# Optimization experiments

Hardware: AMD Instinct MI355X
Metric: run time of the kernel (lower is better)

Reference implementation:

```python
import jax, jax.numpy as jnp
import numpy as np

DIM = 1024
NUM_HEADS = 16
HEAD_DIM = DIM // NUM_HEADS
HIDDEN = 2 * DIM  # swiglu hidden


def rotate_half(x):
    x1, x2 = jnp.split(x, 2, axis=-1)
    return jnp.concatenate((-x2, x1), axis=-1)


def setup_inputs() -> dict:
    key = jax.random.key(0)
    ks = jax.random.split(key, 9)
    s = lambda fan_in: 1.0 / np.sqrt(fan_in)
    x = jax.random.normal(ks[0], (4, 2048, DIM), dtype=jnp.float32)
    qkv_w = jax.random.uniform(ks[1], (3 * DIM, DIM), minval=-s(DIM), maxval=s(DIM))
    proj_w = jax.random.uniform(ks[2], (DIM, DIM), minval=-s(DIM), maxval=s(DIM))
    proj_b = jax.random.uniform(ks[3], (DIM,), minval=-s(DIM), maxval=s(DIM))
    w1_w = jax.random.uniform(ks[4], (HIDDEN, DIM), minval=-s(DIM), maxval=s(DIM))
    w1_b = jnp.zeros((HIDDEN,), jnp.float32)
    w2_w = jax.random.uniform(ks[5], (HIDDEN, DIM), minval=-s(DIM), maxval=s(DIM))
    w2_b = jnp.zeros((HIDDEN,), jnp.float32)
    w3_w = jax.random.uniform(ks[6], (DIM, HIDDEN), minval=-s(HIDDEN), maxval=s(HIDDEN))
    w3_b = jnp.zeros((DIM,), jnp.float32)
    return {"x": x, "qkv_w": qkv_w, "proj_w": proj_w, "proj_b": proj_b,
            "w1_w": w1_w, "w1_b": w1_b, "w2_w": w2_w, "w2_b": w2_b,
            "w3_w": w3_w, "w3_b": w3_b}


def reference(x, qkv_w, proj_w, proj_b, w1_w, w1_b, w2_w, w2_b, w3_w, w3_b):
    B, N, C = x.shape
    H, D = NUM_HEADS, HEAD_DIM
    scale = D ** -0.5
    # QKV projection (no bias)
    qkv = jnp.einsum('bnc,fc->bnf', x, qkv_w).reshape(B, N, 3, H, D)
    qkv = jnp.transpose(qkv, (2, 0, 3, 1, 4))  # [3, B, H, N, D]
    q, k, v = qkv[0], qkv[1], qkv[2]
    # Rotary embeddings
    inv_freq = 1.0 / (10000.0 ** (jnp.arange(0, D, 2, dtype=jnp.float32) / D))
    t = jnp.arange(N, dtype=jnp.float32)
    freqs = jnp.einsum('i,j->ij', t, inv_freq)
    emb = jnp.concatenate((freqs, freqs), axis=-1)[None, None]  # [1,1,N,D]
    cos, sin = jnp.cos(emb), jnp.sin(emb)
    q = q * cos + rotate_half(q) * sin
    k = k * cos + rotate_half(k) * sin
    # Attention (non-causal, as in source)
    attn = jnp.einsum('bhnd,bhmd->bhnm', q, k) * scale
    attn = jax.nn.softmax(attn, axis=-1)
    out = jnp.einsum('bhnm,bhmd->bhnd', attn, v)
    out = jnp.transpose(out, (0, 2, 1, 3)).reshape(B, N, C)
    out = jnp.einsum('bnc,fc->bnf', out, proj_w) + proj_b
    # SwiGLU MLP
    x1 = jnp.einsum('bnc,fc->bnf', out, w1_w) + w1_b
    x2 = jnp.einsum('bnc,fc->bnf', out, w2_w) + w2_b
    hidden = jax.nn.silu(x1) * x2
    return jnp.einsum('bnh,fh->bnf', hidden, w3_w) + w3_b
```

## Files before the change

### kernel.cpp

```cpp
#include <hip/hip_runtime.h>
#include <hip/hip_bf16.h>
#include <math.h>


#define SEQ     2048
#define BATCH   4
#define NH      16
#define CDIM    1024
#define MROWS   8192

typedef __bf16 bf16x8 __attribute__((ext_vector_type(8)));
typedef float  floatx4 __attribute__((ext_vector_type(4)));
typedef float  floatx16 __attribute__((ext_vector_type(16)));
typedef unsigned int u32;

__device__ __forceinline__ unsigned short f2bf(float f) {
    __bf16 h = (__bf16)f;
    return __builtin_bit_cast(unsigned short, h);
}
__device__ __forceinline__ float fexp2(float x) {
    float r; asm("v_exp_f32 %0, %1" : "=v"(r) : "v"(x)); return r;
}
__device__ __forceinline__ float frcp(float x) {
    float r; asm("v_rcp_f32 %0, %1" : "=v"(r) : "v"(x)); return r;
}
__device__ __forceinline__ u32 cvtpk(float lo, float hi) {
    u32 w; asm("v_cvt_pk_bf16_f32 %0, %1, %2" : "=v"(w) : "v"(lo), "v"(hi));
    return w;
}
__device__ __forceinline__ floatx4 mfma16(bf16x8 a, bf16x8 b, floatx4 c) {
    return __builtin_amdgcn_mfma_f32_16x16x32_bf16(a, b, c, 0, 0, 0);
}
__device__ __forceinline__ floatx16 mfma32(bf16x8 a, bf16x8 b, floatx16 c) {
    return __builtin_amdgcn_mfma_f32_32x32x16_bf16(a, b, c, 0, 0, 0);
}
__device__ __forceinline__ void gld16(void* lds, const void* g) {
    __builtin_amdgcn_global_load_lds(
        (const __attribute__((address_space(1))) u32*)g,
        (__attribute__((address_space(3))) u32*)lds, 16, 0, 0);
}
__device__ __forceinline__ void wait_vm0_barrier() {
    asm volatile("s_waitcnt vmcnt(0)" ::: "memory");
    __builtin_amdgcn_s_barrier();
    __builtin_amdgcn_sched_barrier(0);
}
__device__ __forceinline__ void raw_barrier() {
    __builtin_amdgcn_s_barrier();
    __builtin_amdgcn_sched_barrier(0);
}

template <int OUTMODE, bool BIAS>
__global__ __launch_bounds__(256) void mgemm(
    const unsigned short* __restrict__ A,
    const unsigned short* __restrict__ B,
    const float* __restrict__ bias,
    void* __restrict__ C, int ldc,
    int K)
{
    __shared__ __align__(16) unsigned short As[2][128 * 32];
    __shared__ __align__(16) unsigned short Bs[2][128 * 32];

    const int tid  = threadIdx.x;
    const int lane = tid & 63;
    const int wave = tid >> 6;
    const int l16  = lane & 15;
    const int quad = lane >> 4;
    const int wm = (wave >> 1) * 64, wn = (wave & 1) * 64;
    const int bm = blockIdx.y, bn = blockIdx.x;

    const unsigned short* Ag = A + (size_t)(bm * 128) * K;
    const unsigned short* Bg = B + (size_t)(bn * 128) * K;

    const int srow0 = wave * 32 + (lane >> 2);
    const int scol  = (lane & 3) * 8;
    const unsigned short* gA0 = Ag + (size_t)srow0 * K + scol;
    const unsigned short* gA1 = Ag + (size_t)(srow0 + 16) * K + scol;
    const unsigned short* gB0 = Bg + (size_t)srow0 * K + scol;
    const unsigned short* gB1 = Bg + (size_t)(srow0 + 16) * K + scol;

    auto stage = [&](int b, int kt) {
        gld16(&As[b][(wave * 2 + 0) * 512], gA0 + kt);
        gld16(&As[b][(wave * 2 + 1) * 512], gA1 + kt);
        gld16(&Bs[b][(wave * 2 + 0) * 512], gB0 + kt);
        gld16(&Bs[b][(wave * 2 + 1) * 512], gB1 + kt);
    };

    floatx4 acc[4][4] = {};
    const int NK = K >> 5;

    stage(0, 0);
    wait_vm0_barrier();

    for (int i = 0; i < NK; ++i) {
        const int cur = i & 1;
        if (i + 1 < NK) stage(cur ^ 1, (i + 1) * 32);

        bf16x8 af[4], bfr[4];
        #pragma unroll
        for (int mt = 0; mt < 4; ++mt)
            af[mt] = *(const bf16x8*)&As[cur][(wm + mt * 16 + l16) * 32 + quad * 8];
        #pragma unroll
        for (int nt = 0; nt < 4; ++nt)
            bfr[nt] = *(const bf16x8*)&Bs[cur][(wn + nt * 16 + l16) * 32 + quad * 8];
        #pragma unroll
        for (int mt = 0; mt < 4; ++mt)
            #pragma unroll
            for (int nt = 0; nt < 4; ++nt)
                acc[mt][nt] = mfma16(af[mt], bfr[nt], acc[mt][nt]);

        if (i + 1 < NK) wait_vm0_barrier();
        else            raw_barrier();
    }

    #pragma unroll
    for (int nt = 0; nt < 4; ++nt) {
        const int gcol = bn * 128 + wn + nt * 16 + l16;
        const float bv = BIAS ? bias[gcol] : 0.0f;
        #pragma unroll
        for (int mt = 0; mt < 4; ++mt) {
            #pragma unroll
            for (int r = 0; r < 4; ++r) {
                const int grow = bm * 128 + wm + mt * 16 + quad * 4 + r;
                float v = acc[mt][nt][r] + bv;
                if (OUTMODE == 0)
                    ((float*)C)[(size_t)grow * ldc + gcol] = v;
                else
                    ((unsigned short*)C)[(size_t)grow * ldc + gcol] = f2bf(v);
            }
        }
    }
}

__global__ __launch_bounds__(256) void mgemm_glu(
    const unsigned short* __restrict__ A,
    const unsigned short* __restrict__ B1,
    const unsigned short* __restrict__ B2,
    const float* __restrict__ bias1,
    const float* __restrict__ bias2,
    unsigned short* __restrict__ C, int ldc,
    int K)
{
    __shared__ __align__(16) unsigned short As[2][128 * 32];
    __shared__ __align__(16) unsigned short B1s[2][64 * 32];
    __shared__ __align__(16) unsigned short B2s[2][64 * 32];

    const int tid  = threadIdx.x;
    const int lane = tid & 63;
    const int wave = tid >> 6;
    const int l16  = lane & 15;
    const int quad = lane >> 4;
    const int wm = (wave >> 1) * 64, wn = (wave & 1) * 32;
    const int bm = blockIdx.y, bn = blockIdx.x;

    const unsigned short* Ag  = A  + (size_t)(bm * 128) * K;
    const unsigned short* B1g = B1 + (size_t)(bn * 64) * K;
    const unsigned short* B2g = B2 + (size_t)(bn * 64) * K;

    const int arow = wave * 32 + (lane >> 2);
    const int brow = wave * 16 + (lane >> 2);
    const int scol = (lane & 3) * 8;
    const unsigned short* gA0 = Ag  + (size_t)arow * K + scol;
    const unsigned short* gA1 = Ag  + (size_t)(arow + 16) * K + scol;
    const unsigned short* gB1 = B1g + (size_t)brow * K + scol;
    const unsigned short* gB2 = B2g + (size_t)brow * K + scol;

    auto stage = [&](int b, int kt) {
        gld16(&As[b][(wave * 2 + 0) * 512], gA0 + kt);
        gld16(&As[b][(wave * 2 + 1) * 512], gA1 + kt);
        gld16(&B1s[b][wave * 512], gB1 + kt);
        gld16(&B2s[b][wave * 512], gB2 + kt);
    };

    floatx4 acc1[4][2] = {};
    floatx4 acc2[4][2] = {};
    const int NK = K >> 5;

    stage(0, 0);
    wait_vm0_barrier();

    for (int i = 0; i < NK; ++i) {
        const int cur = i & 1;
        if (i + 1 < NK) stage(cur ^ 1, (i + 1) * 32);

        bf16x8 af[4], b1f[2], b2f[2];
        #pragma unroll
        for (int mt = 0; mt < 4; ++mt)
            af[mt] = *(const bf16x8*)&As[cur][(wm + mt * 16 + l16) * 32 + quad * 8];
        #pragma unroll
        for (int nt = 0; nt < 2; ++nt) {
            b1f[nt] = *(const bf16x8*)&B1s[cur][(wn + nt * 16 + l16) * 32 + quad * 8];
            b2f[nt] = *(const bf16x8*)&B2s[cur][(wn + nt * 16 + l16) * 32 + quad * 8];
        }
        #pragma unroll
        for (int mt = 0; mt < 4; ++mt)
            #pragma unroll
            for (int nt = 0; nt < 2; ++nt) {
                acc1[mt][nt] = mfma16(af[mt], b1f[nt], acc1[mt][nt]);
                acc2[mt][nt] = mfma16(af[mt], b2f[nt], acc2[mt][nt]);
            }

        if (i + 1 < NK) wait_vm0_barrier();
        else            raw_barrier();
    }

    #pragma unroll
    for (int nt = 0; nt < 2; ++nt) {
        const int gcol = bn * 64 + wn + nt * 16 + l16;
        const float b1 = bias1[gcol];
        const float b2 = bias2[gcol];
        #pragma unroll
        for (int mt = 0; mt < 4; ++mt) {
            #pragma unroll
            for (int r = 0; r < 4; ++r) {
                const int grow = bm * 128 + wm + mt * 16 + quad * 4 + r;
                const float x1 = acc1[mt][nt][r] + b1;
                const float x2 = acc2[mt][nt][r] + b2;
                const float e = fexp2(x1 * -1.44269504088896f);
                const float v = x1 * frcp(1.0f + e) * x2;
                C[(size_t)grow * ldc + gcol] = f2bf(v);
            }
        }
    }
}

__global__ __launch_bounds__(256) void mgemm_qkv(
    const unsigned short* __restrict__ A,
    const unsigned short* __restrict__ B,
    const float* __restrict__ tab,
    unsigned short* __restrict__ Qb,
    unsigned short* __restrict__ Kb,
    unsigned short* __restrict__ Vtb)
{
    __shared__ __align__(16) unsigned short As[2][128 * 32];
    __shared__ __align__(16) unsigned short Bs[2][128 * 32];

    const int tid  = threadIdx.x;
    const int lane = tid & 63;
    const int wave = tid >> 6;
    const int l16  = lane & 15;
    const int quad = lane >> 4;
    const int wm = (wave >> 1) * 64, wn = (wave & 1) * 64;
    const int bm = blockIdx.y, bn = blockIdx.x;
    const int K = CDIM;

    const unsigned short* Ag = A + (size_t)(bm * 128) * K;
    const unsigned short* Bg = B + (size_t)(bn * 128) * K;

    const int srow0 = wave * 32 + (lane >> 2);
    const int scol  = (lane & 3) * 8;
    const unsigned short* gA0 = Ag + (size_t)srow0 * K + scol;
    const unsigned short* gA1 = Ag + (size_t)(srow0 + 16) * K + scol;
    const unsigned short* gB0 = Bg + (size_t)srow0 * K + scol;
    const unsigned short* gB1 = Bg + (size_t)(srow0 + 16) * K + scol;

    auto stage = [&](int b, int kt) {
        gld16(&As[b][(wave * 2 + 0) * 512], gA0 + kt);
        gld16(&As[b][(wave * 2 + 1) * 512], gA1 + kt);
        gld16(&Bs[b][(wave * 2 + 0) * 512], gB0 + kt);
        gld16(&Bs[b][(wave * 2 + 1) * 512], gB1 + kt);
    };

    floatx4 acc[4][4] = {};
    const int NK = K >> 5;

    stage(0, 0);
    wait_vm0_barrier();

    for (int i = 0; i < NK; ++i) {
        const int cur = i & 1;
        if (i + 1 < NK) stage(cur ^ 1, (i + 1) * 32);

        bf16x8 af[4], bfr[4];
        #pragma unroll
        for (int mt = 0; mt < 4; ++mt)
            af[mt] = *(const bf16x8*)&As[cur][(wm + mt * 16 + l16) * 32 + quad * 8];
        #pragma unroll
        for (int nt = 0; nt < 4; ++nt)
            bfr[nt] = *(const bf16x8*)&Bs[cur][(wn + nt * 16 + l16) * 32 + quad * 8];
        #pragma unroll
        for (int mt = 0; mt < 4; ++mt)
            #pragma unroll
            for (int nt = 0; nt < 4; ++nt)
                acc[mt][nt] = mfma16(af[mt], bfr[nt], acc[mt][nt]);

        if (i + 1 < NK) wait_vm0_barrier();
        else            raw_barrier();
    }

    const int colbase0 = bn * 128;
    const int part = colbase0 >> 10;

    if (part == 2) {
        unsigned short* T = &As[0][0];
        #pragma unroll
        for (int mt = 0; mt < 4; ++mt) {
            __syncthreads();
            #pragma unroll
            for (int nt = 0; nt < 4; ++nt) {
                ushort4 pk;
                pk.x = f2bf(acc[mt][nt][0]); pk.y = f2bf(acc[mt][nt][1]);
                pk.z = f2bf(acc[mt][nt][2]); pk.w = f2bf(acc[mt][nt][3]);
                *(ushort4*)&T[((wave * 64 + nt * 16 + l16) * 16) + quad * 4] = pk;
            }
            __syncthreads();
            const int w2 = tid >> 6, d = tid & 63;
            const int nrow0 = bm * 128 + (w2 >> 1) * 64 + mt * 16;
            const int b = nrow0 >> 11, n0 = nrow0 & 2047;
            const int h2 = ((bn * 128 + (w2 & 1) * 64) & 1023) >> 6;
            unsigned short* dst = Vtb +
                ((size_t)(b * NH + h2) * 64 + d) * 2048 + n0;
            const int tb = (w2 * 64 + d) * 16;
            *(uint4*)dst       = *(const uint4*)&T[tb];
            *(uint4*)(dst + 8) = *(const uint4*)&T[tb + 8];
        }
    } else {
        const float qscale = (part == 0) ? 0.125f * 1.44269504088896f : 1.0f;
        const int h = ((colbase0 + wn) & 1023) >> 6;
        #pragma unroll
        for (int mt = 0; mt < 4; ++mt) {
            #pragma unroll
            for (int r = 0; r < 4; ++r) {
                const int grow = bm * 128 + wm + mt * 16 + quad * 4 + r;
                const int b = grow >> 11, n = grow & 2047;
                unsigned short* dst =
                    (part == 0 ? Qb : Kb) + ((size_t)(b * NH + h) * 2048 + n) * 64;
                #pragma unroll
                for (int nt = 0; nt < 2; ++nt) {
                    const int i = nt * 16 + l16;
                    const float c  = tab[(n * 32 + i) * 2];
                    const float sn = tab[(n * 32 + i) * 2 + 1];
                    const float x1 = acc[mt][nt][r];
                    const float x2v = acc[mt][nt + 2][r];
                    dst[i]      = f2bf((x1 * c - x2v * sn) * qscale);
                    dst[i + 32] = f2bf((x2v * c + x1 * sn) * qscale);
                }
            }
        }
    }
}

__global__ __launch_bounds__(256) void attn_mfma(
    const unsigned short* __restrict__ Qb,
    const unsigned short* __restrict__ Kb,
    const unsigned short* __restrict__ Vtb,
    unsigned short* __restrict__ Ob)
{
    const int bh = blockIdx.x;
    const int qt = blockIdx.y;
    const int tid = threadIdx.x;
    const int lane = tid & 63, wave = tid >> 6;
    const int r32 = lane & 31, hi = lane >> 5;
    const int qrow = wave * 32 + r32;

    __shared__ unsigned short QP[128][72];
    __shared__ unsigned short Ks[64][72];
    __shared__ unsigned short Vs[64][72];

    const unsigned short* Qg = Qb + ((size_t)bh * 2048 + qt * 128) * 64;
    const unsigned short* Kg = Kb + (size_t)bh * 2048 * 64;
    const unsigned short* Vg = Vtb + (size_t)bh * 64 * 2048;

    #pragma unroll
    for (int rep = 0; rep < 4; ++rep) {
        const int c = tid + rep * 256;
        const int r = c >> 3, d0 = (c & 7) * 8;
        *(uint4*)&QP[r][d0] = *(const uint4*)(Qg + (size_t)r * 64 + d0);
    }

    const int c0 = tid, c1 = tid + 256;
    const int kr0 = c0 >> 3, kd0 = (c0 & 7) * 8;
    const int kr1 = c1 >> 3, kd1 = (c1 & 7) * 8;

    uint4 ka0 = *(const uint4*)(Kg + (size_t)kr0 * 64 + kd0);
    uint4 ka1 = *(const uint4*)(Kg + (size_t)kr1 * 64 + kd1);
    uint4 va0 = *(const uint4*)(Vg + (size_t)kr0 * 2048 + kd0);
    uint4 va1 = *(const uint4*)(Vg + (size_t)kr1 * 2048 + kd1);

    __syncthreads();

    bf16x8 bq[4];
    #pragma unroll
    for (int f = 0; f < 4; ++f)
        bq[f] = *(const bf16x8*)&QP[qrow][f * 16 + hi * 8];

    floatx16 o0 = {}, o1 = {};
    float l_acc = 0.0f;

    for (int kt = 0; kt < 32; ++kt) {
        __syncthreads();
        *(uint4*)&Ks[kr0][kd0] = ka0;
        *(uint4*)&Ks[kr1][kd1] = ka1;
        *(uint4*)&Vs[kr0][kd0] = va0;
        *(uint4*)&Vs[kr1][kd1] = va1;
        if (kt + 1 < 32) {
            const size_t nb = (size_t)(kt + 1) * 64;
            ka0 = *(const uint4*)(Kg + (nb + kr0) * 64 + kd0);
            ka1 = *(const uint4*)(Kg + (nb + kr1) * 64 + kd1);
            va0 = *(const uint4*)(Vg + (size_t)kr0 * 2048 + nb + kd0);
            va1 = *(const uint4*)(Vg + (size_t)kr1 * 2048 + nb + kd1);
        }
        __syncthreads();

        #pragma unroll
        for (int t = 0; t < 2; ++t) {
            floatx16 s = {};
            #pragma unroll
            for (int f = 0; f < 4; ++f) {
                const bf16x8 ak = *(const bf16x8*)&Ks[t * 32 + r32][f * 16 + hi * 8];
                s = mfma32(ak, bq[f], s);
            }
            float p[16];
            float rs = 0.0f;
            #pragma unroll
            for (int g = 0; g < 16; ++g) { p[g] = fexp2(s[g]); rs += p[g]; }
            l_acc += rs;
            u32 w0 = cvtpk(p[0], p[1]),   w2 = cvtpk(p[4], p[5]);
            u32 w1 = cvtpk(p[2], p[3]),   w3 = cvtpk(p[6], p[7]);
            u32 w4 = cvtpk(p[8], p[9]),   w6 = cvtpk(p[12], p[13]);
            u32 w5 = cvtpk(p[10], p[11]), w7 = cvtpk(p[14], p[15]);
            asm("v_permlane32_swap_b32 %0, %1" : "+v"(w0), "+v"(w2));
            asm("v_permlane32_swap_b32 %0, %1" : "+v"(w1), "+v"(w3));
            asm("v_permlane32_swap_b32 %0, %1" : "+v"(w4), "+v"(w6));
            asm("v_permlane32_swap_b32 %0, %1" : "+v"(w5), "+v"(w7));
            uint4 u0; u0.x = w0; u0.y = w1; u0.z = w2; u0.w = w3;
            uint4 u1; u1.x = w4; u1.y = w5; u1.z = w6; u1.w = w7;
            const bf16x8 bp0 = __builtin_bit_cast(bf16x8, u0);
            const bf16x8 bp1 = __builtin_bit_cast(bf16x8, u1);
            {
                const int f0 = 2 * t, f1 = 2 * t + 1;
                const bf16x8 av00 = *(const bf16x8*)&Vs[r32][f0 * 16 + hi * 8];
                const bf16x8 av01 = *(const bf16x8*)&Vs[32 + r32][f0 * 16 + hi * 8];
                o0 = mfma32(av00, bp0, o0);
                o1 = mfma32(av01, bp0, o1);
                const bf16x8 av10 = *(const bf16x8*)&Vs[r32][f1 * 16 + hi * 8];
                const bf16x8 av11 = *(const bf16x8*)&Vs[32 + r32][f1 * 16 + hi * 8];
                o0 = mfma32(av10, bp1, o0);
                o1 = mfma32(av11, bp1, o1);
            }
        }
    }

    const float l_tot = l_acc + __shfl_xor(l_acc, 32);
    const float inv = 1.0f / l_tot;
    const int b = bh >> 4, h = bh & 15;
    unsigned short* orow = Ob +
        (size_t)(b * SEQ + qt * 128 + qrow) * CDIM + h * 64;
    #pragma unroll
    for (int u = 0; u < 2; ++u) {
        const floatx16 ov = u ? o1 : o0;
        #pragma unroll
        for (int g = 0; g < 4; ++g) {
            ushort4 pk;
            pk.x = f2bf(ov[4 * g + 0] * inv); pk.y = f2bf(ov[4 * g + 1] * inv);
            pk.z = f2bf(ov[4 * g + 2] * inv); pk.w = f2bf(ov[4 * g + 3] * inv);
            *(ushort4*)(orow + u * 32 + 8 * g + 4 * hi) = pk;
        }
    }
}

__global__ __launch_bounds__(256) void cvt_all(
    const float* __restrict__ x,    const float* __restrict__ qkv,
    const float* __restrict__ proj, const float* __restrict__ w1,
    const float* __restrict__ w2,   const float* __restrict__ w3,
    unsigned short* __restrict__ xb,    unsigned short* __restrict__ qkvb,
    unsigned short* __restrict__ projb, unsigned short* __restrict__ w1b,
    unsigned short* __restrict__ w2b,   unsigned short* __restrict__ w3b)
{
    const size_t i = ((size_t)blockIdx.x * 256 + threadIdx.x) * 4;
    const float* src; unsigned short* dst; size_t off;
    if      (i <  8388608) { src = x;    dst = xb;    off = 0; }
    else if (i < 11534336) { src = qkv;  dst = qkvb;  off = 8388608; }
    else if (i < 12582912) { src = proj; dst = projb; off = 11534336; }
    else if (i < 14680064) { src = w1;   dst = w1b;   off = 12582912; }
    else if (i < 16777216) { src = w2;   dst = w2b;   off = 14680064; }
    else                   { src = w3;   dst = w3b;   off = 16777216; }
    const size_t j = i - off;
    const float4 f = *(const float4*)(src + j);
    ushort4 o; o.x = f2bf(f.x); o.y = f2bf(f.y); o.z = f2bf(f.z); o.w = f2bf(f.w);
    *(ushort4*)(dst + j) = o;
}

__global__ __launch_bounds__(256) void rope_table(float* __restrict__ tab)
{
    const int idx = blockIdx.x * 256 + threadIdx.x;
    const int i = idx & 31, n = idx >> 5;
    const double f = (double)n * pow(10000.0, -(double)(2 * i) / 64.0);
    tab[idx * 2]     = (float)cos(f);
    tab[idx * 2 + 1] = (float)sin(f);
}

extern "C" void kernel_launch(void* const* d_in, const int* in_sizes, int n_in,
                              void* d_out, int out_size, void* d_ws, size_t ws_size,
                              hipStream_t stream)
{
    const float* x      = (const float*)d_in[0];
    const float* qkv_w  = (const float*)d_in[1];
    const float* proj_w = (const float*)d_in[2];
    const float* proj_b = (const float*)d_in[3];
    const float* w1_w   = (const float*)d_in[4];
    const float* w1_b   = (const float*)d_in[5];
    const float* w2_w   = (const float*)d_in[6];
    const float* w2_b   = (const float*)d_in[7];
    const float* w3_w   = (const float*)d_in[8];
    const float* w3_b   = (const float*)d_in[9];
    float* out = (float*)d_out;

    char* ws = (char*)d_ws;
    unsigned short* Qb    = (unsigned short*)(ws);
    unsigned short* Kb    = (unsigned short*)(ws + 16777216);
    unsigned short* Vtb   = (unsigned short*)(ws + 33554432);
    unsigned short* Ob    = (unsigned short*)(ws + 50331648);
    unsigned short* out1b = (unsigned short*)(ws + 67108864);
    unsigned short* w1b   = (unsigned short*)(ws + 83886080);
    unsigned short* w2b   = (unsigned short*)(ws + 88080384);
    unsigned short* w3b   = (unsigned short*)(ws + 92274688);
    unsigned short* projb = (unsigned short*)(ws + 96468992);
    unsigned short* xb    = (unsigned short*)(ws + 98566144);
    unsigned short* wqkvb = (unsigned short*)(ws + 115343360);
    float*          tab   = (float*)(ws + 121634816);
    unsigned short* hid   = (unsigned short*)(ws);

    const dim3 blk(256);

    cvt_all<<<dim3(18432), blk, 0, stream>>>(
        x, qkv_w, proj_w, w1_w, w2_w, w3_w,
        xb, wqkvb, projb, w1b, w2b, w3b);
    rope_table<<<dim3(256), blk, 0, stream>>>(tab);

    mgemm_qkv<<<dim3(24, 64), blk, 0, stream>>>(xb, wqkvb, tab, Qb, Kb, Vtb);
    attn_mfma<<<dim3(BATCH * NH, SEQ / 128), blk, 0, stream>>>(Qb, Kb, Vtb, Ob);
    mgemm<1, true><<<dim3(8, 64), blk, 0, stream>>>(
        Ob, projb, proj_b, out1b, CDIM, CDIM);
    mgemm_glu<<<dim3(32, 64), blk, 0, stream>>>(
        out1b, w1b, w2b, w1_b, w2_b, hid, 2048, CDIM);
    mgemm<0, true><<<dim3(8, 64), blk, 0, stream>>>(
        hid, w3b, w3_b, out, CDIM, 2048);
}
```

Before: 479.9 us.

## Load GEMM B operand fragments directly from global into registers, bypassing LDS

In the three GEMM kernels (generic, SwiGLU, QKV), the weight (B) tiles are no longer staged through shared memory. Each wave now loads its own MFMA B fragments straight from global memory into registers, prefetched one k-step ahead, while A stays double-buffered in LDS. This removes half the LDS traffic and LDS footprint, which may allow more blocks per CU. The cost is that each B element is now fetched by both waves sharing the same wn instead of once per block, the 16-byte loads per lane are strided by K and so less coalesced, and prefetch registers grow.

```diff
diff --git a/kernel.cpp b/kernel.cpp
--- a/kernel.cpp
+++ b/kernel.cpp
@@ -58,7 +58,6 @@
     int K)
 {
     __shared__ __align__(16) unsigned short As[2][128 * 32];
-    __shared__ __align__(16) unsigned short Bs[2][128 * 32];
 
     const int tid  = threadIdx.x;
     const int lane = tid & 63;
@@ -75,41 +74,54 @@
     const int scol  = (lane & 3) * 8;
     const unsigned short* gA0 = Ag + (size_t)srow0 * K + scol;
     const unsigned short* gA1 = Ag + (size_t)(srow0 + 16) * K + scol;
-    const unsigned short* gB0 = Bg + (size_t)srow0 * K + scol;
-    const unsigned short* gB1 = Bg + (size_t)(srow0 + 16) * K + scol;
-
-    auto stage = [&](int b, int kt) {
+
+    auto stageA = [&](int b, int kt) {
         gld16(&As[b][(wave * 2 + 0) * 512], gA0 + kt);
         gld16(&As[b][(wave * 2 + 1) * 512], gA1 + kt);
-        gld16(&Bs[b][(wave * 2 + 0) * 512], gB0 + kt);
-        gld16(&Bs[b][(wave * 2 + 1) * 512], gB1 + kt);
     };
+
+    const unsigned short* gBf[4];
+    #pragma unroll
+    for (int nt = 0; nt < 4; ++nt)
+        gBf[nt] = Bg + (size_t)(wn + nt * 16 + l16) * K + quad * 8;
 
     floatx4 acc[4][4] = {};
     const int NK = K >> 5;
 
-    stage(0, 0);
+    stageA(0, 0);
+    bf16x8 bcur[4];
+    #pragma unroll
+    for (int nt = 0; nt < 4; ++nt)
+        bcur[nt] = *(const bf16x8*)(gBf[nt]);
     wait_vm0_barrier();
 
     for (int i = 0; i < NK; ++i) {
         const int cur = i & 1;
-        if (i + 1 < NK) stage(cur ^ 1, (i + 1) * 32);
-
-        bf16x8 af[4], bfr[4];
+        bf16x8 bnxt[4];
+        if (i + 1 < NK) {
+            stageA(cur ^ 1, (i + 1) * 32);
+            #pragma unroll
+            for (int nt = 0; nt < 4; ++nt)
+                bnxt[nt] = *(const bf16x8*)(gBf[nt] + (i + 1) * 32);
+        }
+
+        bf16x8 af[4];
         #pragma unroll
         for (int mt = 0; mt < 4; ++mt)
             af[mt] = *(const bf16x8*)&As[cur][(wm + mt * 16 + l16) * 32 + quad * 8];
         #pragma unroll
-        for (int nt = 0; nt < 4; ++nt)
-            bfr[nt] = *(const bf16x8*)&Bs[cur][(wn + nt * 16 + l16) * 32 + quad * 8];
-        #pragma unroll
         for (int mt = 0; mt < 4; ++mt)
             #pragma unroll
             for (int nt = 0; nt < 4; ++nt)
-                acc[mt][nt] = mfma16(af[mt], bfr[nt], acc[mt][nt]);
-
-        if (i + 1 < NK) wait_vm0_barrier();
-        else            raw_barrier();
+                acc[mt][nt] = mfma16(af[mt], bcur[nt], acc[mt][nt]);
+
+        if (i + 1 < NK) {
+            wait_vm0_barrier();
+            #pragma unroll
+            for (int nt = 0; nt < 4; ++nt) bcur[nt] = bnxt[nt];
+        } else {
+            raw_barrier();
+        }
     }
 
     #pragma unroll
@@ -141,8 +153,6 @@
     int K)
 {
     __shared__ __align__(16) unsigned short As[2][128 * 32];
-    __shared__ __align__(16) unsigned short B1s[2][64 * 32];
-    __shared__ __align__(16) unsigned short B2s[2][64 * 32];
 
     const int tid  = threadIdx.x;
     const int lane = tid & 63;
@@ -157,50 +167,67 @@
     const unsigned short* B2g = B2 + (size_t)(bn * 64) * K;
 
     const int arow = wave * 32 + (lane >> 2);
-    const int brow = wave * 16 + (lane >> 2);
     const int scol = (lane & 3) * 8;
-    const unsigned short* gA0 = Ag  + (size_t)arow * K + scol;
-    const unsigned short* gA1 = Ag  + (size_t)(arow + 16) * K + scol;
-    const unsigned short* gB1 = B1g + (size_t)brow * K + scol;
-    const unsigned short* gB2 = B2g + (size_t)brow * K + scol;
-
-    auto stage = [&](int b, int kt) {
+    const unsigned short* gA0 = Ag + (size_t)arow * K + scol;
+    const unsigned short* gA1 = Ag + (size_t)(arow + 16) * K + scol;
+
+    auto stageA = [&](int b, int kt) {
         gld16(&As[b][(wave * 2 + 0) * 512], gA0 + kt);
         gld16(&As[b][(wave * 2 + 1) * 512], gA1 + kt);
-        gld16(&B1s[b][wave * 512], gB1 + kt);
-        gld16(&B2s[b][wave * 512], gB2 + kt);
     };
+
+    const unsigned short* gB1f[2];
+    const unsigned short* gB2f[2];
+    #pragma unroll
+    for (int nt = 0; nt < 2; ++nt) {
+        gB1f[nt] = B1g + (size_t)(wn + nt * 16 + l16) * K + quad * 8;
+        gB2f[nt] = B2g + (size_t)(wn + nt * 16 + l16) * K + quad * 8;
+    }
 
     floatx4 acc1[4][2] = {};
     floatx4 acc2[4][2] = {};
     const int NK = K >> 5;
 
-    stage(0, 0);
+    stageA(0, 0);
+    bf16x8 b1c[2], b2c[2];
+    #pragma unroll
+    for (int nt = 0; nt < 2; ++nt) {
+        b1c[nt] = *(const bf16x8*)(gB1f[nt]);
+        b2c[nt] = *(const bf16x8*)(gB2f[nt]);
+    }
     wait_vm0_barrier();
 
     for (int i = 0; i < NK; ++i) {
         const int cur = i & 1;
-        if (i + 1 < NK) stage(cur ^ 1, (i + 1) * 32);
-
-        bf16x8 af[4], b1f[2], b2f[2];
+        bf16x8 b1n[2], b2n[2];
+        if (i + 1 < NK) {
+            stageA(cur ^ 1, (i + 1) * 32);
+            #pragma unroll
+            for (int nt = 0; nt < 2; ++nt) {
+                b1n[nt] = *(const bf16x8*)(gB1f[nt] + (i + 1) * 32);
+                b2n[nt] = *(const bf16x8*)(gB2f[nt] + (i + 1) * 32);
+            }
+        }
+
+        bf16x8 af[4];
         #pragma unroll
         for (int mt = 0; mt < 4; ++mt)
             af[mt] = *(const bf16x8*)&As[cur][(wm + mt * 16 + l16) * 32 + quad * 8];
         #pragma unroll
-        for (int nt = 0; nt < 2; ++nt) {
-            b1f[nt] = *(const bf16x8*)&B1s[cur][(wn + nt * 16 + l16) * 32 + quad * 8];
-            b2f[nt] = *(const bf16x8*)&B2s[cur][(wn + nt * 16 + l16) * 32 + quad * 8];
-        }
-        #pragma unroll
         for (int mt = 0; mt < 4; ++mt)
             #pragma unroll
             for (int nt = 0; nt < 2; ++nt) {
-                acc1[mt][nt] = mfma16(af[mt], b1f[nt], acc1[mt][nt]);
-                acc2[mt][nt] = mfma16(af[mt], b2f[nt], acc2[mt][nt]);
-            }
-
-        if (i + 1 < NK) wait_vm0_barrier();
-        else            raw_barrier();
+                acc1[mt][nt] = mfma16(af[mt], b1c[nt], acc1[mt][nt]);
+                acc2[mt][nt] = mfma16(af[mt], b2c[nt], acc2[mt][nt]);
+            }
+
+        if (i + 1 < NK) {
+            wait_vm0_barrier();
+            #pragma unroll
+            for (int nt = 0; nt < 2; ++nt) { b1c[nt] = b1n[nt]; b2c[nt] = b2n[nt]; }
+        } else {
+            raw_barrier();
+        }
     }
 
     #pragma unroll
@@ -232,7 +259,6 @@
     unsigned short* __restrict__ Vtb)
 {
     __shared__ __align__(16) unsigned short As[2][128 * 32];
-    __shared__ __align__(16) unsigned short Bs[2][128 * 32];
 
     const int tid  = threadIdx.x;
     const int lane = tid & 63;
@@ -250,41 +276,54 @@
     const int scol  = (lane & 3) * 8;
     const unsigned short* gA0 = Ag + (size_t)srow0 * K + scol;
     const unsigned short* gA1 = Ag + (size_t)(srow0 + 16) * K + scol;
-    const unsigned short* gB0 = Bg + (size_t)srow0 * K + scol;
-    const unsigned short* gB1 = Bg + (size_t)(srow0 + 16) * K + scol;
-
-    auto stage = [&](int b, int kt) {
+
+    auto stageA = [&](int b, int kt) {
         gld16(&As[b][(wave * 2 + 0) * 512], gA0 + kt);
         gld16(&As[b][(wave * 2 + 1) * 512], gA1 + kt);
-        gld16(&Bs[b][(wave * 2 + 0) * 512], gB0 + kt);
-        gld16(&Bs[b][(wave * 2 + 1) * 512], gB1 + kt);
     };
+
+    const unsigned short* gBf[4];
+    #pragma unroll
+    for (int nt = 0; nt < 4; ++nt)
+        gBf[nt] = Bg + (size_t)(wn + nt * 16 + l16) * K + quad * 8;
 
     floatx4 acc[4][4] = {};
     const int NK = K >> 5;
 
-    stage(0, 0);
+    stageA(0, 0);
+    bf16x8 bcur[4];
+    #pragma unroll
+    for (int nt = 0; nt < 4; ++nt)
+        bcur[nt] = *(const bf16x8*)(gBf[nt]);
     wait_vm0_barrier();
 
     for (int i = 0; i < NK; ++i) {
         const int cur = i & 1;
-        if (i + 1 < NK) stage(cur ^ 1, (i + 1) * 32);
-
-        bf16x8 af[4], bfr[4];
+        bf16x8 bnxt[4];
+        if (i + 1 < NK) {
+            stageA(cur ^ 1, (i + 1) * 32);
+            #pragma unroll
+            for (int nt = 0; nt < 4; ++nt)
+                bnxt[nt] = *(const bf16x8*)(gBf[nt] + (i + 1) * 32);
+        }
+
+        bf16x8 af[4];
         #pragma unroll
         for (int mt = 0; mt < 4; ++mt)
             af[mt] = *(const bf16x8*)&As[cur][(wm + mt * 16 + l16) * 32 + quad * 8];
         #pragma unroll
-        for (int nt = 0; nt < 4; ++nt)
-            bfr[nt] = *(const bf16x8*)&Bs[cur][(wn + nt * 16 + l16) * 32 + quad * 8];
-        #pragma unroll
         for (int mt = 0; mt < 4; ++mt)
             #pragma unroll
             for (int nt = 0; nt < 4; ++nt)
-                acc[mt][nt] = mfma16(af[mt], bfr[nt], acc[mt][nt]);
-
-        if (i + 1 < NK) wait_vm0_barrier();
-        else            raw_barrier();
+                acc[mt][nt] = mfma16(af[mt], bcur[nt], acc[mt][nt]);
+
+        if (i + 1 < NK) {
+            wait_vm0_barrier();
+            #pragma unroll
+            for (int nt = 0; nt < 4; ++nt) bcur[nt] = bnxt[nt];
+        } else {
+            raw_barrier();
+        }
     }
 
     const int colbase0 = bn * 128;
```

Result: slower. 576.8 us (+20.2%).

## Triple-buffer LDS staging in GEMM kernels with two-tile prefetch

Applied to the files above, without the earlier changes.

Moves the three bf16 MFMA GEMM kernels (generic, SwiGLU and QKV) from double to triple LDS buffering. Each loop iteration now prefetches two K-tiles ahead and waits with vmcnt(4), so only the older tile's loads must land before the barrier. The goal is to hide more global-load latency behind MFMA work. In exchange, LDS use per block rises by half, which may lower occupancy, and the final iteration's barrier is dropped.

```diff
diff --git a/kernel.cpp b/kernel.cpp
--- a/kernel.cpp
+++ b/kernel.cpp
@@ -39,12 +39,13 @@
         (const __attribute__((address_space(1))) u32*)g,
         (__attribute__((address_space(3))) u32*)lds, 16, 0, 0);
 }
+__device__ __forceinline__ void wait_vm4_barrier() {
+    asm volatile("s_waitcnt vmcnt(4)" ::: "memory");
+    __builtin_amdgcn_s_barrier();
+    __builtin_amdgcn_sched_barrier(0);
+}
 __device__ __forceinline__ void wait_vm0_barrier() {
     asm volatile("s_waitcnt vmcnt(0)" ::: "memory");
-    __builtin_amdgcn_s_barrier();
-    __builtin_amdgcn_sched_barrier(0);
-}
-__device__ __forceinline__ void raw_barrier() {
     __builtin_amdgcn_s_barrier();
     __builtin_amdgcn_sched_barrier(0);
 }
@@ -57,8 +58,8 @@
     void* __restrict__ C, int ldc,
     int K)
 {
-    __shared__ __align__(16) unsigned short As[2][128 * 32];
-    __shared__ __align__(16) unsigned short Bs[2][128 * 32];
+    __shared__ __align__(16) unsigned short As[3][128 * 32];
+    __shared__ __align__(16) unsigned short Bs[3][128 * 32];
 
     const int tid  = threadIdx.x;
     const int lane = tid & 63;
@@ -89,11 +90,12 @@
     const int NK = K >> 5;
 
     stage(0, 0);
-    wait_vm0_barrier();
+    stage(1, 32);
+    wait_vm4_barrier();
 
     for (int i = 0; i < NK; ++i) {
-        const int cur = i & 1;
-        if (i + 1 < NK) stage(cur ^ 1, (i + 1) * 32);
+        const int cur = i % 3;
+        if (i + 2 < NK) stage((i + 2) % 3, (i + 2) * 32);
 
         bf16x8 af[4], bfr[4];
         #pragma unroll
@@ -108,8 +110,8 @@
             for (int nt = 0; nt < 4; ++nt)
                 acc[mt][nt] = mfma16(af[mt], bfr[nt], acc[mt][nt]);
 
-        if (i + 1 < NK) wait_vm0_barrier();
-        else            raw_barrier();
+        if (i + 2 < NK)      wait_vm4_barrier();
+        else if (i + 1 < NK) wait_vm0_barrier();
     }
 
     #pragma unroll
@@ -140,9 +142,9 @@
     unsigned short* __restrict__ C, int ldc,
     int K)
 {
-    __shared__ __align__(16) unsigned short As[2][128 * 32];
-    __shared__ __align__(16) unsigned short B1s[2][64 * 32];
-    __shared__ __align__(16) unsigned short B2s[2][64 * 32];
+    __shared__ __align__(16) unsigned short As[3][128 * 32];
+    __shared__ __align__(16) unsigned short B1s[3][64 * 32];
+    __shared__ __align__(16) unsigned short B2s[3][64 * 32];
 
     const int tid  = threadIdx.x;
     const int lane = tid & 63;
@@ -176,11 +178,12 @@
     const int NK = K >> 5;
 
     stage(0, 0);
-    wait_vm0_barrier();
+    stage(1, 32);
+    wait_vm4_barrier();
 
     for (int i = 0; i < NK; ++i) {
-        const int cur = i & 1;
-        if (i + 1 < NK) stage(cur ^ 1, (i + 1) * 32);
+        const int cur = i % 3;
+        if (i + 2 < NK) stage((i + 2) % 3, (i + 2) * 32);
 
         bf16x8 af[4], b1f[2], b2f[2];
         #pragma unroll
@@ -199,8 +202,8 @@
                 acc2[mt][nt] = mfma16(af[mt], b2f[nt], acc2[mt][nt]);
             }
 
-        if (i + 1 < NK) wait_vm0_barrier();
-        else            raw_barrier();
+        if (i + 2 < NK)      wait_vm4_barrier();
+        else if (i + 1 < NK) wait_vm0_barrier();
     }
 
     #pragma unroll
@@ -231,8 +234,8 @@
     unsigned short* __restrict__ Kb,
     unsigned short* __restrict__ Vtb)
 {
-    __shared__ __align__(16) unsigned short As[2][128 * 32];
-    __shared__ __align__(16) unsigned short Bs[2][128 * 32];
+    __shared__ __align__(16) unsigned short As[3][128 * 32];
+    __shared__ __align__(16) unsigned short Bs[3][128 * 32];
 
     const int tid  = threadIdx.x;
     const int lane = tid & 63;
@@ -264,11 +267,12 @@
     const int NK = K >> 5;
 
     stage(0, 0);
-    wait_vm0_barrier();
+    stage(1, 32);
+    wait_vm4_barrier();
 
     for (int i = 0; i < NK; ++i) {
-        const int cur = i & 1;
-        if (i + 1 < NK) stage(cur ^ 1, (i + 1) * 32);
+        const int cur = i % 3;
+        if (i + 2 < NK) stage((i + 2) % 3, (i + 2) * 32);
 
         bf16x8 af[4], bfr[4];
         #pragma unroll
@@ -283,8 +287,8 @@
             for (int nt = 0; nt < 4; ++nt)
                 acc[mt][nt] = mfma16(af[mt], bfr[nt], acc[mt][nt]);
 
-        if (i + 1 < NK) wait_vm0_barrier();
-        else            raw_barrier();
+        if (i + 2 < NK)      wait_vm4_barrier();
+        else if (i + 1 < NK) wait_vm0_barrier();
     }
 
     const int colbase0 = bn * 128;
```

Result: no change. 478.5 us (-0.3%).
